# Optimization experiments

Measured on AMD Instinct MI355X. Metric: run time of the kernel, lower is better.

The kernel has to match this reference:

```python
import jax, jax.numpy as jnp
import numpy as np

N = 50000      # nodes
E = 1600000    # edges (before self loops)
G = 64         # graphs in batch
DIN = 128
HID = 64
H = 4
NEG_SLOPE = 0.2
BN_EPS = 1e-5


def setup_inputs() -> dict:
    key = jax.random.key(0)
    ks = jax.random.split(key, 32)
    p = lambda i, shape: 0.1 * jax.random.normal(ks[i], shape, dtype=jnp.float32)
    inp = {
        "x": jax.random.normal(ks[0], (N, DIN), dtype=jnp.float32),
        "edge_index": jax.random.randint(ks[1], (2, E), 0, N),
        "batch": jnp.sort(jax.random.randint(ks[2], (N,), 0, G)),
        # GAT layer 1: DIN -> HID x H heads (concat)
        "W1": p(3, (DIN, H * HID)),
        "att_src1": p(4, (H, HID)),
        "att_dst1": p(5, (H, HID)),
        "bias1": p(6, (H * HID,)),
        "bn1_g": jnp.ones((H * HID,), jnp.float32),
        "bn1_b": jnp.zeros((H * HID,), jnp.float32),
        "bn1_m": p(7, (H * HID,)),
        "bn1_v": jnp.ones((H * HID,), jnp.float32),
        # GAT layer 2: H*HID -> HID, 1 head
        "W2": p(8, (H * HID, HID)),
        "att_src2": p(9, (1, HID)),
        "att_dst2": p(10, (1, HID)),
        "bias2": p(11, (HID,)),
        "bn2_g": jnp.ones((HID,), jnp.float32),
        "bn2_b": jnp.zeros((HID,), jnp.float32),
        "bn2_m": p(12, (HID,)),
        "bn2_v": jnp.ones((HID,), jnp.float32),
        # classifier
        "Wc1": p(13, (HID, HID)),
        "bc1": p(14, (HID,)),
        "Wc2": p(15, (HID, 2)),
        "bc2": p(16, (2,)),
    }
    return inp


def _gat_layer(x, src, dst, W, a_src, a_dst, bias, heads, n):
    # x: [n, F_in]; src/dst: [E'] (self loops included)
    c = W.shape[1] // heads
    xw = (x @ W).reshape(n, heads, c)                       # [n, H, C]
    alpha_s = jnp.sum(xw * a_src, axis=-1)                  # [n, H]
    alpha_d = jnp.sum(xw * a_dst, axis=-1)                  # [n, H]
    e = alpha_s[src] + alpha_d[dst]                         # [E', H]
    e = jnp.where(e >= 0, e, NEG_SLOPE * e)                 # leaky relu
    # softmax over incoming edges of each dst node
    m = jax.ops.segment_max(e, dst, num_segments=n)         # [n, H]
    ex = jnp.exp(e - m[dst])
    denom = jax.ops.segment_sum(ex, dst, num_segments=n)    # [n, H]
    w = ex / (denom[dst] + 1e-16)                           # [E', H]
    out = jax.ops.segment_sum(xw[src] * w[:, :, None], dst, num_segments=n)
    return out.reshape(n, heads * c) + bias


def _bn_eval(x, g, b, m, v):
    return (x - m) * (g / jnp.sqrt(v + BN_EPS)) + b


def reference(x, edge_index, batch,
              W1, att_src1, att_dst1, bias1, bn1_g, bn1_b, bn1_m, bn1_v,
              W2, att_src2, att_dst2, bias2, bn2_g, bn2_b, bn2_m, bn2_v,
              Wc1, bc1, Wc2, bc2):
    n = x.shape[0]
    loops = jnp.arange(n, dtype=edge_index.dtype)
    src = jnp.concatenate([edge_index[0], loops])  # PyG GATConv adds self loops
    dst = jnp.concatenate([edge_index[1], loops])

    h = _gat_layer(x, src, dst, W1, att_src1, att_dst1, bias1, H, n)
    h = jax.nn.relu(_bn_eval(h, bn1_g, bn1_b, bn1_m, bn1_v))
    # residual skipped: dims (256) vs x (128) mismatch -> not added, as in torch code

    h2 = _gat_layer(h, src, dst, W2, att_src2, att_dst2, bias2, 1, n)
    h2 = jax.nn.relu(_bn_eval(h2, bn2_g, bn2_b, bn2_m, bn2_v))
    # residual skipped: 64 vs 256 mismatch

    # global mean pool over each graph
    sums = jax.ops.segment_sum(h2, batch, num_segments=G)
    cnt = jax.ops.segment_sum(jnp.ones((n,), h2.dtype), batch, num_segments=G)
    graph_repr = sums / jnp.maximum(cnt, 1.0)[:, None]      # [G, HID]

    hc = jax.nn.relu(graph_repr @ Wc1 + bc1)
    logits = hc @ Wc2 + bc2
    return jax.nn.log_softmax(logits, axis=1)
```

## Files before the change

### kernel.cpp

```cpp
#include <hip/hip_runtime.h>

#define NEG_SLOPE 0.2f
#define CAP1 224
#define CAP2 224
#define CAPB 5120
#define EPB  16384
#define OVFCAP 65536

typedef short bf16x8 __attribute__((ext_vector_type(8)));
typedef float f32x4  __attribute__((ext_vector_type(4)));
typedef float f32x2  __attribute__((ext_vector_type(2)));

static __device__ __forceinline__ float u16f(unsigned short u){
  union { unsigned int i; float f; } v; v.i = ((unsigned int)u) << 16; return v.f;
}
static __device__ __forceinline__ unsigned short f2u16(float f){
  union { float f; unsigned int i; } v; v.f = f;
  unsigned int r = (v.i + 0x7FFFu + ((v.i >> 16) & 1u)) >> 16;
  return (unsigned short)r;
}
static __device__ __forceinline__ unsigned char f2fp8(float f){
  int w = __builtin_amdgcn_cvt_pk_fp8_f32(f, f, 0, false);
  return (unsigned char)(w & 0xFF);
}
static __device__ __forceinline__ float fp82f(unsigned char b){
  f32x2 d = __builtin_amdgcn_cvt_pk_f32_fp8((int)b, false);
  return d[0];
}
static __device__ __forceinline__ float wsum(float v){
  #pragma unroll
  for (int o = 32; o > 0; o >>= 1) v += __shfl_xor(v, o, 64);
  return v;
}
static __device__ __forceinline__ float qsum(float v){
  #pragma unroll
  for (int o = 1; o < 16; o <<= 1) v += __shfl_xor(v, o, 64);
  return v;
}
static __device__ __forceinline__ float lrelu(float e){
  return e >= 0.f ? e : NEG_SLOPE * e;
}

__global__ __launch_bounds__(256) void k_zero(int* __restrict__ p, int nwords){
  int i = blockIdx.x * 256 + threadIdx.x;
  if (i < nwords) p[i] = 0;
}

__global__ __launch_bounds__(256) void k_cvt(const float* __restrict__ x,
                                             unsigned short* __restrict__ xb, int n4){
  int i = blockIdx.x * 256 + threadIdx.x;
  if (i >= n4) return;
  float4 f = ((const float4*)x)[i];
  ushort4 u;
  u.x = f2u16(f.x); u.y = f2u16(f.y); u.z = f2u16(f.z); u.w = f2u16(f.w);
  ((ushort4*)xb)[i] = u;
}

__global__ __launch_bounds__(256) void k_pack1(const float* __restrict__ W1,
                                               unsigned short* __restrict__ B1p){
  int idx = blockIdx.x * 256 + threadIdx.x;
  if (idx >= 4*16*64*8) return;
  int j = idx & 7, lane = (idx >> 3) & 63, nt = (idx >> 9) & 15, kc = idx >> 13;
  int k = kc*32 + (lane >> 4)*8 + j;
  int n = nt*16 + (lane & 15);
  B1p[idx] = f2u16(W1[k*256 + n]);
}

__global__ __launch_bounds__(256) void k_pack2(const float* __restrict__ W2,
                                               unsigned short* __restrict__ B2p){
  int idx = blockIdx.x * 256 + threadIdx.x;
  if (idx >= 8*4*64*8) return;
  int j = idx & 7, lane = (idx >> 3) & 63, nt = (idx >> 9) & 3, kc = idx >> 11;
  int k = kc*32 + (lane >> 4)*8 + j;
  int n = nt*16 + (lane & 15);
  B2p[idx] = f2u16(W2[k*64 + n]);
}

__global__ __launch_bounds__(256) void k_gemm1m(
    const unsigned short* __restrict__ xb, const bf16x8* __restrict__ B1p,
    const float* __restrict__ asrc, const float* __restrict__ adst,
    unsigned char* __restrict__ xw1, float* __restrict__ oas, float* __restrict__ oad,
    int N)
{
  __shared__ unsigned short xs[64][136];
  int t = threadIdx.x;
  int m0 = blockIdx.x * 64;
  #pragma unroll
  for (int i = 0; i < 4; ++i){
    int flat = t + i*256;
    int r = flat >> 4, c8 = flat & 15;
    uint4 v = make_uint4(0,0,0,0);
    if (m0 + r < N) v = *(const uint4*)(xb + (size_t)(m0 + r)*128 + c8*8);
    *(uint4*)&xs[r][c8*8] = v;
  }
  __syncthreads();
  int w = t >> 6, l = t & 63;
  int quad = l >> 4, ml = l & 15;

  f32x4 acc[16];
  #pragma unroll
  for (int i = 0; i < 16; ++i){ acc[i][0]=0.f; acc[i][1]=0.f; acc[i][2]=0.f; acc[i][3]=0.f; }

  #pragma unroll
  for (int kc = 0; kc < 4; ++kc){
    bf16x8 a = *(const bf16x8*)&xs[w*16 + ml][kc*32 + quad*8];
    #pragma unroll
    for (int nt = 0; nt < 16; ++nt){
      bf16x8 b = B1p[(kc*16 + nt)*64 + l];
      acc[nt] = __builtin_amdgcn_mfma_f32_16x16x32_bf16(a, b, acc[nt], 0, 0, 0);
    }
  }

  float as_h[4][4], ad_h[4][4];
  #pragma unroll
  for (int h = 0; h < 4; ++h)
    #pragma unroll
    for (int r = 0; r < 4; ++r){ as_h[h][r] = 0.f; ad_h[h][r] = 0.f; }
  #pragma unroll
  for (int nt = 0; nt < 16; ++nt){
    float vs = asrc[nt*16 + ml], vd = adst[nt*16 + ml];
    int h = nt >> 2;
    #pragma unroll
    for (int r = 0; r < 4; ++r){
      as_h[h][r] += acc[nt][r] * vs;
      ad_h[h][r] += acc[nt][r] * vd;
    }
  }
  #pragma unroll
  for (int h = 0; h < 4; ++h)
    #pragma unroll
    for (int r = 0; r < 4; ++r){ as_h[h][r] = qsum(as_h[h][r]); ad_h[h][r] = qsum(ad_h[h][r]); }

  int baserow = m0 + w*16 + quad*4;
  if (ml == 0){
    #pragma unroll
    for (int r = 0; r < 4; ++r){
      int node = baserow + r;
      if (node < N){
        *(float4*)(oas + (size_t)node*4) = make_float4(as_h[0][r], as_h[1][r], as_h[2][r], as_h[3][r]);
        *(float4*)(oad + (size_t)node*4) = make_float4(ad_h[0][r], ad_h[1][r], ad_h[2][r], ad_h[3][r]);
      }
    }
  }
  #pragma unroll
  for (int r = 0; r < 4; ++r){
    int node = baserow + r;
    if (node >= N) continue;
    #pragma unroll
    for (int nt = 0; nt < 16; ++nt)
      xw1[(size_t)node*256 + nt*16 + ml] = f2fp8(acc[nt][r]);
  }
}

__global__ __launch_bounds__(256) void k_gemm2m(
    const unsigned short* __restrict__ h1, const bf16x8* __restrict__ B2p,
    const float* __restrict__ asrc, const float* __restrict__ adst,
    unsigned char* __restrict__ xw2, float* __restrict__ oas, float* __restrict__ oad,
    int N)
{
  __shared__ unsigned short ys[64][264];
  int t = threadIdx.x;
  int m0 = blockIdx.x * 64;
  #pragma unroll
  for (int i = 0; i < 8; ++i){
    int flat = t + i*256;
    int r = flat >> 5, c8 = flat & 31;
    uint4 v = make_uint4(0,0,0,0);
    if (m0 + r < N) v = *(const uint4*)(h1 + (size_t)(m0 + r)*256 + c8*8);
    *(uint4*)&ys[r][c8*8] = v;
  }
  __syncthreads();
  int w = t >> 6, l = t & 63;
  int quad = l >> 4, ml = l & 15;

  f32x4 acc[4];
  #pragma unroll
  for (int i = 0; i < 4; ++i){ acc[i][0]=0.f; acc[i][1]=0.f; acc[i][2]=0.f; acc[i][3]=0.f; }

  #pragma unroll
  for (int kc = 0; kc < 8; ++kc){
    bf16x8 a = *(const bf16x8*)&ys[w*16 + ml][kc*32 + quad*8];
    #pragma unroll
    for (int nt = 0; nt < 4; ++nt){
      bf16x8 b = B2p[(kc*4 + nt)*64 + l];
      acc[nt] = __builtin_amdgcn_mfma_f32_16x16x32_bf16(a, b, acc[nt], 0, 0, 0);
    }
  }

  float as_p[4] = {0,0,0,0}, ad_p[4] = {0,0,0,0};
  #pragma unroll
  for (int nt = 0; nt < 4; ++nt){
    float vs = asrc[nt*16 + ml], vd = adst[nt*16 + ml];
    #pragma unroll
    for (int r = 0; r < 4; ++r){
      as_p[r] += acc[nt][r] * vs;
      ad_p[r] += acc[nt][r] * vd;
    }
  }
  #pragma unroll
  for (int r = 0; r < 4; ++r){ as_p[r] = qsum(as_p[r]); ad_p[r] = qsum(ad_p[r]); }

  int baserow = m0 + w*16 + quad*4;
  if (ml == 0){
    #pragma unroll
    for (int r = 0; r < 4; ++r){
      int node = baserow + r;
      if (node < N){ oas[node] = as_p[r]; oad[node] = ad_p[r]; }
    }
  }
  #pragma unroll
  for (int r = 0; r < 4; ++r){
    int node = baserow + r;
    if (node >= N) continue;
    #pragma unroll
    for (int nt = 0; nt < 4; ++nt)
      xw2[(size_t)node*64 + nt*16 + ml] = f2fp8(acc[nt][r]);
  }
}

__global__ __launch_bounds__(256) void k_scan1(const int* __restrict__ count,
                                               int* __restrict__ ro, int* __restrict__ bsum, int N){
  __shared__ int sd[256];
  int t = threadIdx.x, b = blockIdx.x, i = b*256 + t;
  int v = (i < N) ? count[i] : 0;
  sd[t] = v; __syncthreads();
  for (int o = 1; o < 256; o <<= 1){
    int x = (t >= o) ? sd[t - o] : 0;
    __syncthreads();
    sd[t] += x;
    __syncthreads();
  }
  if (i < N) ro[i] = sd[t] - v;
  if (t == 255) bsum[b] = sd[255];
}

__global__ __launch_bounds__(256) void k_scan2(int* __restrict__ bsum, int nb){
  __shared__ int sd[256];
  int t = threadIdx.x;
  int v = (t < nb) ? bsum[t] : 0;
  sd[t] = v; __syncthreads();
  for (int o = 1; o < 256; o <<= 1){
    int x = (t >= o) ? sd[t - o] : 0;
    __syncthreads();
    sd[t] += x;
    __syncthreads();
  }
  if (t < nb) bsum[t] = sd[t] - v;
}

__global__ __launch_bounds__(256) void k_scan3(int* __restrict__ ro,
                                               const int* __restrict__ bsum, int N, int ET){
  int b = blockIdx.x, t = threadIdx.x, i = b*256 + t;
  if (i < N) ro[i] += bsum[b];
  if (b == 0 && t == 0) ro[N] = ET;
}

__global__ __launch_bounds__(1024) void k_binscat(const int* __restrict__ ei,
                                                  int* __restrict__ bincur,
                                                  int* __restrict__ binbuf,
                                                  int* __restrict__ ovfcnt,
                                                  int2* __restrict__ ovfbuf,
                                                  int E, int ET, int NB){
  __shared__ int lhist[512];
  __shared__ int lbase[512];
  __shared__ int lcur[512];
  int t = threadIdx.x;
  int base = blockIdx.x * EPB;
  for (int i = t; i < 512; i += 1024){ lhist[i] = 0; lcur[i] = 0; }
  __syncthreads();

  int myb[16], mypay[16];
  #pragma unroll
  for (int k = 0; k < 16; ++k){
    int i = base + t + k*1024;
    int b = -1, pay = 0;
    if (i < ET){
      int s, d;
      if (i < E){ s = ei[i]; d = ei[E + i]; }
      else      { s = i - E; d = i - E; }
      b = d >> 7;
      pay = ((d & 127) << 16) | s;
      atomicAdd(&lhist[b], 1);
    }
    myb[k] = b; mypay[k] = pay;
  }
  __syncthreads();

  for (int i = t; i < NB; i += 1024){
    int h = lhist[i];
    if (h > 0) lbase[i] = atomicAdd(&bincur[i * 16], h);
  }
  __syncthreads();

  #pragma unroll
  for (int k = 0; k < 16; ++k){
    int b = myb[k];
    if (b < 0) continue;
    int pos = lbase[b] + atomicAdd(&lcur[b], 1);
    if (pos < CAPB){
      binbuf[(size_t)b * CAPB + pos] = mypay[k];
    } else {
      int d = (b << 7) | (mypay[k] >> 16);
      int s = mypay[k] & 0xFFFF;
      int idx = atomicAdd(ovfcnt, 1);
      if (idx < OVFCAP) ovfbuf[idx] = make_int2(d, s);
    }
  }
}

__global__ __launch_bounds__(256) void k_cnt(const int* __restrict__ bincur,
                                             const int* __restrict__ binbuf,
                                             int* __restrict__ count, int N){
  __shared__ int lcnt[128];
  int b = blockIdx.x, t = threadIdx.x;
  int base = b << 7;
  int wn = N - base; if (wn > 128) wn = 128;
  if (wn <= 0) return;
  for (int i = t; i < wn; i += 256) lcnt[i] = 0;
  __syncthreads();
  int total = bincur[b * 16];
  int cnt = total < CAPB ? total : CAPB;
  const int* buf = binbuf + (size_t)b * CAPB;
  for (int i = t; i < cnt; i += 256) atomicAdd(&lcnt[buf[i] >> 16], 1);
  __syncthreads();
  for (int i = t; i < wn; i += 256) count[base + i] = lcnt[i];
}

__global__ __launch_bounds__(256) void k_cntovf(const int* __restrict__ ovfcnt,
                                                const int2* __restrict__ ovfbuf,
                                                int* __restrict__ count){
  int n = ovfcnt[0]; if (n > OVFCAP) n = OVFCAP;
  for (int i = blockIdx.x*256 + threadIdx.x; i < n; i += gridDim.x*256)
    atomicAdd(&count[ovfbuf[i].x], 1);
}

__global__ __launch_bounds__(256) void k_ovfscat(const int* __restrict__ ovfcnt,
                                                 const int2* __restrict__ ovfbuf,
                                                 const int* __restrict__ ro,
                                                 int* __restrict__ cursor,
                                                 int* __restrict__ csr){
  int n = ovfcnt[0]; if (n > OVFCAP) n = OVFCAP;
  for (int i = blockIdx.x*256 + threadIdx.x; i < n; i += gridDim.x*256){
    int d = ovfbuf[i].x, s = ovfbuf[i].y;
    int pos = atomicAdd(&cursor[d], 1);
    csr[ro[d + 1] - 1 - pos] = s;
  }
}

__global__ __launch_bounds__(256) void k_binsort(const int* __restrict__ bincur,
                                                 const int* __restrict__ binbuf,
                                                 const int* __restrict__ ro,
                                                 int* __restrict__ csr, int N){
  __shared__ int rolocal[129];
  __shared__ int lcnt[128];
  __shared__ int stage[CAPB];
  int b = blockIdx.x, t = threadIdx.x;
  int base = b << 7;
  int wn = N - base; if (wn > 128) wn = 128;
  if (wn <= 0) return;
  for (int i = t; i <= wn; i += 256) rolocal[i] = ro[base + i];
  for (int i = t; i < wn; i += 256) lcnt[i] = 0;
  __syncthreads();
  int rostart = rolocal[0];
  int seglen = rolocal[wn] - rostart;
  int total = bincur[b * 16];
  int cnt = total < CAPB ? total : CAPB;
  bool ovf = (seglen > CAPB) || (total > CAPB);
  const int* buf = binbuf + (size_t)b * CAPB;

  if (!ovf){
    for (int i = t; i < cnt; i += 256){
      int u = buf[i];
      int s = u & 0xFFFF, ld = u >> 16;
      int r = atomicAdd(&lcnt[ld], 1);
      stage[rolocal[ld] - rostart + r] = s;
    }
    __syncthreads();
    for (int i = t; i < seglen; i += 256) csr[rostart + i] = stage[i];
  } else {
    for (int i = t; i < cnt; i += 256){
      int u = buf[i];
      int s = u & 0xFFFF, ld = u >> 16;
      int r = atomicAdd(&lcnt[ld], 1);
      csr[rolocal[ld] + r] = s;
    }
  }
}

__global__ __launch_bounds__(256) void k_edge1(
    const int* __restrict__ ro, const int* __restrict__ cs,
    const unsigned char* __restrict__ xw1,
    const float* __restrict__ pas, const float* __restrict__ pad,
    const float* __restrict__ bias1,
    const float* __restrict__ g1, const float* __restrict__ b1,
    const float* __restrict__ m1, const float* __restrict__ v1,
    unsigned short* __restrict__ h1, int N)
{
  __shared__ float wt[4][CAP1][5];
  int t = threadIdx.x, w = t >> 6, lane = t & 63;
  int n = blockIdx.x * 4 + w;
  if (n >= N) return;
  int beg = ro[n], end = ro[n + 1], deg = end - beg;
  const float4 adv = *(const float4*)(pad + (size_t)n * 4);
  const bool fits = (deg <= CAP1);

  float s0 = 0.f, s1 = 0.f, s2 = 0.f, s3 = 0.f;
  for (int j = lane; j < deg; j += 64){
    int s = cs[beg + j];
    float4 a = *(const float4*)(pas + (size_t)s * 4);
    float e0 = __expf(lrelu(a.x + adv.x));
    float e1 = __expf(lrelu(a.y + adv.y));
    float e2 = __expf(lrelu(a.z + adv.z));
    float e3 = __expf(lrelu(a.w + adv.w));
    if (fits){
      wt[w][j][0] = e0; wt[w][j][1] = e1;
      wt[w][j][2] = e2; wt[w][j][3] = e3;
      wt[w][j][4] = __int_as_float(s << 8);
    }
    s0 += e0; s1 += e1; s2 += e2; s3 += e3;
  }
  s0 = wsum(s0); s1 = wsum(s1); s2 = wsum(s2); s3 = wsum(s3);

  int head = lane >> 4;
  float invh = 1.f / ((head == 0 ? s0 : head == 1 ? s1 : head == 2 ? s2 : s3) + 1e-16f);
  float aa   = head == 0 ? adv.x : head == 1 ? adv.y : head == 2 ? adv.z : adv.w;

  float a0 = 0.f, a1 = 0.f, a2 = 0.f, a3 = 0.f;
  if (fits){
    for (int j = 0; j < deg; ++j){
      float wv = wt[w][j][head] * invh;
      int off = __float_as_int(wt[w][j][4]);
      int u = *(const int*)(xw1 + off + lane * 4);
      f32x2 lo = __builtin_amdgcn_cvt_pk_f32_fp8(u, false);
      f32x2 hi = __builtin_amdgcn_cvt_pk_f32_fp8(u, true);
      a0 += wv * lo[0]; a1 += wv * lo[1];
      a2 += wv * hi[0]; a3 += wv * hi[1];
    }
  } else {
    for (int j = 0; j < deg; ++j){
      int s = cs[beg + j];
      float wv = __expf(lrelu(pas[(size_t)s * 4 + head] + aa)) * invh;
      int u = *(const int*)(xw1 + (size_t)s * 256 + lane * 4);
      f32x2 lo = __builtin_amdgcn_cvt_pk_f32_fp8(u, false);
      f32x2 hi = __builtin_amdgcn_cvt_pk_f32_fp8(u, true);
      a0 += wv * lo[0]; a1 += wv * lo[1];
      a2 += wv * hi[0]; a3 += wv * hi[1];
    }
  }

  float accv[4] = {a0, a1, a2, a3};
  ushort4 outv;
  unsigned short* po = (unsigned short*)&outv;
  int j0 = lane * 4;
  #pragma unroll
  for (int i = 0; i < 4; ++i){
    int j = j0 + i;
    float o  = accv[i] + bias1[j];
    float sc = g1[j] * rsqrtf(v1[j] + 1e-5f);
    float res = (o - m1[j]) * sc + b1[j];
    po[i] = f2u16(fmaxf(res, 0.f));
  }
  *(ushort4*)(h1 + (size_t)n * 256 + j0) = outv;
}

__global__ __launch_bounds__(256) void k_edge2(
    const int* __restrict__ ro, const int* __restrict__ cs,
    const unsigned char* __restrict__ xw2,
    const float* __restrict__ pas, const float* __restrict__ pad,
    const float* __restrict__ bias2,
    const float* __restrict__ g2, const float* __restrict__ b2,
    const float* __restrict__ m2, const float* __restrict__ v2,
    float* __restrict__ h2, int N)
{
  __shared__ float wt[4][CAP2][2];
  int t = threadIdx.x, w = t >> 6, lane = t & 63;
  int n = blockIdx.x * 4 + w;
  if (n >= N) return;
  int beg = ro[n], end = ro[n + 1], deg = end - beg;
  float adv = pad[n];
  const bool fits = (deg <= CAP2);

  float dh = 0.f;
  for (int j = lane; j < deg; j += 64){
    int s = cs[beg + j];
    float e = __expf(lrelu(pas[s] + adv));
    if (fits){
      wt[w][j][0] = e;
      wt[w][j][1] = __int_as_float(s << 6);
    }
    dh += e;
  }
  dh = wsum(dh);
  float inv = 1.f / (dh + 1e-16f);

  float acc = 0.f;
  if (fits){
    for (int j = 0; j < deg; ++j){
      float wv = wt[w][j][0] * inv;
      int off = __float_as_int(wt[w][j][1]);
      acc += wv * fp82f(xw2[off + lane]);
    }
  } else {
    for (int j = 0; j < deg; ++j){
      int s = cs[beg + j];
      float wv = __expf(lrelu(pas[s] + adv)) * inv;
      acc += wv * fp82f(xw2[(size_t)s * 64 + lane]);
    }
  }

  float o  = acc + bias2[lane];
  float sc = g2[lane] * rsqrtf(v2[lane] + 1e-5f);
  h2[(size_t)n * 64 + lane] = fmaxf((o - m2[lane]) * sc + b2[lane], 0.f);
}

__global__ __launch_bounds__(256) void k_pool(
    const float* __restrict__ h2, const int* __restrict__ batch,
    float* __restrict__ pool, int N)
{
  int g = blockIdx.x;
  int t = threadIdx.x, c = t & 63, w = t >> 6;
  int lo = 0, hi = N;
  while (lo < hi){ int mid = (lo + hi) >> 1; if (batch[mid] < g) lo = mid + 1; else hi = mid; }
  int lo2 = lo, hi2 = N;
  while (lo2 < hi2){ int mid = (lo2 + hi2) >> 1; if (batch[mid] < g + 1) lo2 = mid + 1; else hi2 = mid; }
  float s = 0.f;
  for (int r = lo + w; r < lo2; r += 4) s += h2[(size_t)r * 64 + c];
  __shared__ float sd[4][64];
  sd[w][c] = s;
  __syncthreads();
  if (w == 0){
    float tot = sd[0][c] + sd[1][c] + sd[2][c] + sd[3][c];
    float cntf = (float)(lo2 - lo);
    pool[g * 64 + c] = tot / fmaxf(cntf, 1.f);
  }
}

__global__ __launch_bounds__(64) void k_final(
    const float* __restrict__ pool,
    const float* __restrict__ Wc1, const float* __restrict__ bc1,
    const float* __restrict__ Wc2, const float* __restrict__ bc2,
    float* __restrict__ out)
{
  int g = blockIdx.x, c = threadIdx.x;
  __shared__ float gr[64];
  gr[c] = pool[g * 64 + c];
  __syncthreads();
  float a = bc1[c];
  for (int k = 0; k < 64; ++k) a += gr[k] * Wc1[k * 64 + c];
  float hc = fmaxf(a, 0.f);
  float p0 = hc * Wc2[c * 2 + 0];
  float p1 = hc * Wc2[c * 2 + 1];
  p0 = wsum(p0); p1 = wsum(p1);
  if (c == 0){
    float l0 = p0 + bc2[0];
    float l1 = p1 + bc2[1];
    float mx = fmaxf(l0, l1);
    float lse = mx + logf(expf(l0 - mx) + expf(l1 - mx));
    out[g * 2 + 0] = l0 - lse;
    out[g * 2 + 1] = l1 - lse;
  }
}

extern "C" void kernel_launch(void* const* d_in, const int* in_sizes, int n_in,
                              void* d_out, int out_size, void* d_ws, size_t ws_size,
                              hipStream_t stream)
{
  const float* x     = (const float*)d_in[0];
  const int*   ei    = (const int*)d_in[1];
  const int*   batch = (const int*)d_in[2];
  const float* W1    = (const float*)d_in[3];
  const float* asrc1 = (const float*)d_in[4];
  const float* adst1 = (const float*)d_in[5];
  const float* bias1 = (const float*)d_in[6];
  const float* bn1g  = (const float*)d_in[7];
  const float* bn1b  = (const float*)d_in[8];
  const float* bn1m  = (const float*)d_in[9];
  const float* bn1v  = (const float*)d_in[10];
  const float* W2    = (const float*)d_in[11];
  const float* asrc2 = (const float*)d_in[12];
  const float* adst2 = (const float*)d_in[13];
  const float* bias2 = (const float*)d_in[14];
  const float* bn2g  = (const float*)d_in[15];
  const float* bn2b  = (const float*)d_in[16];
  const float* bn2m  = (const float*)d_in[17];
  const float* bn2v  = (const float*)d_in[18];
  const float* Wc1   = (const float*)d_in[19];
  const float* bc1   = (const float*)d_in[20];
  const float* Wc2   = (const float*)d_in[21];
  const float* bc2   = (const float*)d_in[22];
  float* out = (float*)d_out;

  const int N  = in_sizes[0] / 128;
  const int E  = in_sizes[1] / 2;
  const int ET = E + N;
  const int NB = (N + 127) >> 7;

  char* p = (char*)d_ws;
  auto take = [&](size_t bytes) -> void* {
    void* q = (void*)p;
    p += ((bytes + 255) & ~(size_t)255);
    return q;
  };
  int*   cursor = (int*)  take((size_t)N * 4);
  int*   bincur = (int*)  take((size_t)NB * 16 * 4);
  int*   ovfcnt = (int*)  take(256);
  size_t zbytes = (size_t)(p - (char*)d_ws);
  int*   count  = (int*)  take((size_t)N * 4);
  float* pool   = (float*)take(64 * 64 * 4);
  int*   ro     = (int*)  take((size_t)(N + 1) * 4);
  int*   bsum   = (int*)  take(1024);
  float* as1    = (float*)take((size_t)N * 16);
  float* ad1    = (float*)take((size_t)N * 16);
  float* as2    = (float*)take((size_t)N * 4);
  float* ad2    = (float*)take((size_t)N * 4);
  unsigned char*  xw1 = (unsigned char*) take((size_t)N * 256);
  unsigned short* h1  = (unsigned short*)take((size_t)N * 256 * 2);
  float* h2     = (float*)take((size_t)N * 64 * 4);
  int*   csr    = (int*)  take((size_t)ET * 4);
  int*   binbuf = (int*)  take((size_t)NB * CAPB * 4);
  int2*  ovfbuf = (int2*) take((size_t)OVFCAP * 8);
  unsigned short* B1p = (unsigned short*)take(32768 * 2);
  unsigned short* B2p = (unsigned short*)take(16384 * 2);
  unsigned short* xb  = (unsigned short*)h2;
  unsigned char*  xw2 = xw1;
  (void)n_in; (void)ws_size; (void)out_size;

  int zw = (int)(zbytes / 4);
  k_zero<<<dim3((zw + 255) / 256), dim3(256), 0, stream>>>((int*)d_ws, zw);
  int n4 = N * 32;
  k_cvt<<<dim3((n4 + 255) / 256), dim3(256), 0, stream>>>(x, xb, n4);
  k_pack1<<<dim3(128), dim3(256), 0, stream>>>(W1, B1p);
  k_pack2<<<dim3(64), dim3(256), 0, stream>>>(W2, B2p);
  k_binscat<<<dim3((ET + EPB - 1) / EPB), dim3(1024), 0, stream>>>(ei, bincur, binbuf,
                                                                   ovfcnt, ovfbuf, E, ET, NB);
  k_cnt<<<dim3(NB), dim3(256), 0, stream>>>(bincur, binbuf, count, N);
  k_cntovf<<<dim3(8), dim3(256), 0, stream>>>(ovfcnt, ovfbuf, count);
  int nb = (N + 255) / 256;
  k_scan1<<<dim3(nb), dim3(256), 0, stream>>>(count, ro, bsum, N);
  k_scan2<<<dim3(1), dim3(256), 0, stream>>>(bsum, nb);
  k_scan3<<<dim3(nb), dim3(256), 0, stream>>>(ro, bsum, N, ET);
  k_binsort<<<dim3(NB), dim3(256), 0, stream>>>(bincur, binbuf, ro, csr, N);
  k_ovfscat<<<dim3(8), dim3(256), 0, stream>>>(ovfcnt, ovfbuf, ro, cursor, csr);
  k_gemm1m<<<dim3((N + 63) / 64), dim3(256), 0, stream>>>(xb, (const bf16x8*)B1p,
                                                          asrc1, adst1, xw1, as1, ad1, N);
  k_edge1<<<dim3((N + 3) / 4), dim3(256), 0, stream>>>(ro, csr, xw1, as1, ad1,
                                                       bias1, bn1g, bn1b, bn1m, bn1v, h1, N);
  k_gemm2m<<<dim3((N + 63) / 64), dim3(256), 0, stream>>>(h1, (const bf16x8*)B2p,
                                                          asrc2, adst2, xw2, as2, ad2, N);
  k_edge2<<<dim3((N + 3) / 4), dim3(256), 0, stream>>>(ro, csr, xw2, as2, ad2,
                                                       bias2, bn2g, bn2b, bn2m, bn2v, h2, N);
  k_pool<<<dim3(64), dim3(256), 0, stream>>>(h2, batch, pool, N);
  k_final<<<dim3(64), dim3(64), 0, stream>>>(pool, Wc1, bc1, Wc2, bc2, out);
}
```

Baseline: 370.9 us.

## Process four edges per wave iteration with wide loads in GAT aggregation

```diff
diff --git a/kernel.cpp b/kernel.cpp
--- a/kernel.cpp
+++ b/kernel.cpp
@@ -421,22 +421,61 @@
   }
   s0 = wsum(s0); s1 = wsum(s1); s2 = wsum(s2); s3 = wsum(s3);
 
-  int head = lane >> 4;
-  float invh = 1.f / ((head == 0 ? s0 : head == 1 ? s1 : head == 2 ? s2 : s3) + 1e-16f);
-  float aa   = head == 0 ? adv.x : head == 1 ? adv.y : head == 2 ? adv.z : adv.w;
-
-  float a0 = 0.f, a1 = 0.f, a2 = 0.f, a3 = 0.f;
   if (fits){
-    for (int j = 0; j < deg; ++j){
-      float wv = wt[w][j][head] * invh;
-      int off = __float_as_int(wt[w][j][4]);
-      int u = *(const int*)(xw1 + off + lane * 4);
-      f32x2 lo = __builtin_amdgcn_cvt_pk_f32_fp8(u, false);
-      f32x2 hi = __builtin_amdgcn_cvt_pk_f32_fp8(u, true);
-      a0 += wv * lo[0]; a1 += wv * lo[1];
-      a2 += wv * hi[0]; a3 += wv * hi[1];
+    float i0 = 1.f/(s0+1e-16f), i1 = 1.f/(s1+1e-16f), i2 = 1.f/(s2+1e-16f), i3 = 1.f/(s3+1e-16f);
+    for (int j = lane; j < deg; j += 64){
+      wt[w][j][0] *= i0; wt[w][j][1] *= i1;
+      wt[w][j][2] *= i2; wt[w][j][3] *= i3;
+    }
+
+    int sub = lane & 15, quad = lane >> 4;
+    int hh = sub >> 2;
+    float acc[16];
+    #pragma unroll
+    for (int i = 0; i < 16; ++i) acc[i] = 0.f;
+
+    for (int j0 = 0; j0 < deg; j0 += 4){
+      int j = j0 + quad;
+      if (j < deg){
+        float wv = wt[w][j][hh];
+        int off = __float_as_int(wt[w][j][4]);
+        uint4 u = *(const uint4*)(xw1 + off + sub * 16);
+        f32x2 p;
+        p = __builtin_amdgcn_cvt_pk_f32_fp8((int)u.x, false); acc[0] += wv*p[0]; acc[1] += wv*p[1];
+        p = __builtin_amdgcn_cvt_pk_f32_fp8((int)u.x, true);  acc[2] += wv*p[0]; acc[3] += wv*p[1];
+        p = __builtin_amdgcn_cvt_pk_f32_fp8((int)u.y, false); acc[4] += wv*p[0]; acc[5] += wv*p[1];
+        p = __builtin_amdgcn_cvt_pk_f32_fp8((int)u.y, true);  acc[6] += wv*p[0]; acc[7] += wv*p[1];
+        p = __builtin_amdgcn_cvt_pk_f32_fp8((int)u.z, false); acc[8] += wv*p[0]; acc[9] += wv*p[1];
+        p = __builtin_amdgcn_cvt_pk_f32_fp8((int)u.z, true);  acc[10] += wv*p[0]; acc[11] += wv*p[1];
+        p = __builtin_amdgcn_cvt_pk_f32_fp8((int)u.w, false); acc[12] += wv*p[0]; acc[13] += wv*p[1];
+        p = __builtin_amdgcn_cvt_pk_f32_fp8((int)u.w, true);  acc[14] += wv*p[0]; acc[15] += wv*p[1];
+      }
+    }
+    #pragma unroll
+    for (int i = 0; i < 16; ++i){
+      acc[i] += __shfl_xor(acc[i], 16, 64);
+      acc[i] += __shfl_xor(acc[i], 32, 64);
+    }
+    if (quad == 0){
+      #pragma unroll
+      for (int gq = 0; gq < 4; ++gq){
+        ushort4 ov;
+        unsigned short* po = (unsigned short*)&ov;
+        #pragma unroll
+        for (int i2 = 0; i2 < 4; ++i2){
+          int c = sub*16 + gq*4 + i2;
+          float o  = acc[gq*4 + i2] + bias1[c];
+          float sc = g1[c] * rsqrtf(v1[c] + 1e-5f);
+          po[i2] = f2u16(fmaxf((o - m1[c]) * sc + b1[c], 0.f));
+        }
+        *(ushort4*)(h1 + (size_t)n * 256 + sub*16 + gq*4) = ov;
+      }
     }
   } else {
+    int head = lane >> 4;
+    float invh = 1.f / ((head == 0 ? s0 : head == 1 ? s1 : head == 2 ? s2 : s3) + 1e-16f);
+    float aa   = head == 0 ? adv.x : head == 1 ? adv.y : head == 2 ? adv.z : adv.w;
+    float a0 = 0.f, a1 = 0.f, a2 = 0.f, a3 = 0.f;
     for (int j = 0; j < deg; ++j){
       int s = cs[beg + j];
       float wv = __expf(lrelu(pas[(size_t)s * 4 + head] + aa)) * invh;
@@ -446,21 +485,19 @@
       a0 += wv * lo[0]; a1 += wv * lo[1];
       a2 += wv * hi[0]; a3 += wv * hi[1];
     }
-  }
-
-  float accv[4] = {a0, a1, a2, a3};
-  ushort4 outv;
-  unsigned short* po = (unsigned short*)&outv;
-  int j0 = lane * 4;
-  #pragma unroll
-  for (int i = 0; i < 4; ++i){
-    int j = j0 + i;
-    float o  = accv[i] + bias1[j];
-    float sc = g1[j] * rsqrtf(v1[j] + 1e-5f);
-    float res = (o - m1[j]) * sc + b1[j];
-    po[i] = f2u16(fmaxf(res, 0.f));
-  }
-  *(ushort4*)(h1 + (size_t)n * 256 + j0) = outv;
+    float accv[4] = {a0, a1, a2, a3};
+    ushort4 outv;
+    unsigned short* po = (unsigned short*)&outv;
+    int j0 = lane * 4;
+    #pragma unroll
+    for (int i = 0; i < 4; ++i){
+      int j = j0 + i;
+      float o  = accv[i] + bias1[j];
+      float sc = g1[j] * rsqrtf(v1[j] + 1e-5f);
+      po[i] = f2u16(fmaxf((o - m1[j]) * sc + b1[j], 0.f));
+    }
+    *(ushort4*)(h1 + (size_t)n * 256 + j0) = outv;
+  }
 }
 
 __global__ __launch_bounds__(256) void k_edge2(
@@ -493,24 +530,51 @@
   dh = wsum(dh);
   float inv = 1.f / (dh + 1e-16f);
 
-  float acc = 0.f;
   if (fits){
-    for (int j = 0; j < deg; ++j){
-      float wv = wt[w][j][0] * inv;
-      int off = __float_as_int(wt[w][j][1]);
-      acc += wv * fp82f(xw2[off + lane]);
+    for (int j = lane; j < deg; j += 64) wt[w][j][0] *= inv;
+
+    int sub = lane & 15, quad = lane >> 4;
+    float acc[4] = {0.f, 0.f, 0.f, 0.f};
+    for (int j0 = 0; j0 < deg; j0 += 4){
+      int j = j0 + quad;
+      if (j < deg){
+        float wv = wt[w][j][0];
+        int off = __float_as_int(wt[w][j][1]);
+        unsigned int u = *(const unsigned int*)(xw2 + off + sub * 4);
+        f32x2 lo = __builtin_amdgcn_cvt_pk_f32_fp8((int)u, false);
+        f32x2 hi = __builtin_amdgcn_cvt_pk_f32_fp8((int)u, true);
+        acc[0] += wv * lo[0]; acc[1] += wv * lo[1];
+        acc[2] += wv * hi[0]; acc[3] += wv * hi[1];
+      }
+    }
+    #pragma unroll
+    for (int i = 0; i < 4; ++i){
+      acc[i] += __shfl_xor(acc[i], 16, 64);
+      acc[i] += __shfl_xor(acc[i], 32, 64);
+    }
+    if (quad == 0){
+      float4 ov;
+      float* po = (float*)&ov;
+      #pragma unroll
+      for (int i2 = 0; i2 < 4; ++i2){
+        int c = sub*4 + i2;
+        float o  = acc[i2] + bias2[c];
+        float sc = g2[c] * rsqrtf(v2[c] + 1e-5f);
+        po[i2] = fmaxf((o - m2[c]) * sc + b2[c], 0.f);
+      }
+      *(float4*)(h2 + (size_t)n * 64 + sub*4) = ov;
     }
   } else {
+    float acc = 0.f;
     for (int j = 0; j < deg; ++j){
       int s = cs[beg + j];
       float wv = __expf(lrelu(pas[s] + adv)) * inv;
       acc += wv * fp82f(xw2[(size_t)s * 64 + lane]);
     }
-  }
-
-  float o  = acc + bias2[lane];
-  float sc = g2[lane] * rsqrtf(v2[lane] + 1e-5f);
-  h2[(size_t)n * 64 + lane] = fmaxf((o - m2[lane]) * sc + b2[lane], 0.f);
+    float o  = acc + bias2[lane];
+    float sc = g2[lane] * rsqrtf(v2[lane] + 1e-5f);
+    h2[(size_t)n * 64 + lane] = fmaxf((o - m2[lane]) * sc + b2[lane], 0.f);
+  }
 }
 
 __global__ __launch_bounds__(256) void k_pool(
```

New measurement: 390.9 us. 5.4% more time.
